# Kernel optimization log

Hardware: AMD Instinct MI355X
Metric: run time of the kernel (lower is better)

Reference implementation:

```python
import jax, jax.numpy as jnp
import numpy as np

B, S, E = 2, 2048, 1024
H = 16
HD = E // H  # 64


def setup_inputs() -> dict:
    key = jax.random.key(0)
    ks = jax.random.split(key, 9)
    sc = 1.0 / np.sqrt(E)
    return {
        "X": jax.random.normal(ks[0], (B, S, E), jnp.float32),
        "Wq": jax.random.normal(ks[1], (E, E), jnp.float32) * sc,
        "bq": jax.random.normal(ks[2], (E,), jnp.float32) * sc,
        "Wk": jax.random.normal(ks[3], (E, E), jnp.float32) * sc,
        "bk": jax.random.normal(ks[4], (E,), jnp.float32) * sc,
        "Wv": jax.random.normal(ks[5], (E, E), jnp.float32) * sc,
        "bv": jax.random.normal(ks[6], (E,), jnp.float32) * sc,
        "Wo": jax.random.normal(ks[7], (E, E), jnp.float32) * sc,
        "bo": jax.random.normal(ks[8], (E,), jnp.float32) * sc,
    }


def reference(X, Wq, bq, Wk, bk, Wv, bv, Wo, bo):
    b, s, e = X.shape
    # torch Linear: x @ W.T + b (weights stored (out, in))
    Q = X @ Wq.T + bq
    K = X @ Wk.T + bk
    V = X @ Wv.T + bv
    # (b, s, E) -> (b, H, s, HD)
    Q = Q.reshape(b, s, H, HD).transpose(0, 2, 1, 3)
    K = K.reshape(b, s, H, HD).transpose(0, 2, 1, 3)
    V = V.reshape(b, s, H, HD).transpose(0, 2, 1, 3)
    scores = jnp.einsum("bhqd,bhkd->bhqk", Q, K) / np.sqrt(HD).astype(np.float32)
    attn = jax.nn.softmax(scores, axis=-1)
    ctx = jnp.einsum("bhqk,bhkd->bhqd", attn, V)  # (b, H, s, HD)
    # Faithful to original: reshape (b,H,s,HD) -> (b,s,E) WITHOUT permuting heads back
    ctx = ctx.reshape(b, s, e)
    return ctx @ Wo.T + bo
```

## Files before the change

kernel.cpp:

```cpp
#include <hip/hip_runtime.h>


typedef __bf16 bf16x8 __attribute__((ext_vector_type(8)));
typedef __bf16 bf16x4 __attribute__((ext_vector_type(4)));
typedef float f32x4 __attribute__((ext_vector_type(4)));
typedef unsigned short ushort_t;

#define S_LEN 2048
#define E_DIM 1024
#define H_NUM 16
#define HD_DIM 64

__device__ __forceinline__ ushort_t f2bf(float f) {
  union { float f; unsigned u; } v; v.f = f;
  unsigned u = v.u;
  unsigned r = (u + 0x7FFFu + ((u >> 16) & 1u)) >> 16;
  return (ushort_t)r;
}

#define GLDS16(gp, lp)                                              \
  __builtin_amdgcn_global_load_lds(                                 \
      (const __attribute__((address_space(1))) unsigned int*)(gp),  \
      (__attribute__((address_space(3))) unsigned int*)(lp), 16, 0, 0)

__global__ __launch_bounds__(256) void cvt_all(
    const float* __restrict__ X, const float* __restrict__ Wq,
    const float* __restrict__ Wk, const float* __restrict__ Wv,
    const float* __restrict__ Wo, ushort_t* __restrict__ Xbf,
    ushort_t* __restrict__ Wqkv, ushort_t* __restrict__ Wob) {
  int i = blockIdx.x * 256 + threadIdx.x;
  const float* src;
  ushort_t* dst;
  int off;
  if (i < 1048576) {
    src = X; dst = Xbf; off = i;
  } else if (i < 1310720) {
    src = Wq; dst = Wqkv; off = i - 1048576;
  } else if (i < 1572864) {
    src = Wk; dst = Wqkv + (1 << 20); off = i - 1310720;
  } else if (i < 1835008) {
    src = Wv; dst = Wqkv + (2 << 20); off = i - 1572864;
  } else {
    src = Wo; dst = Wob; off = i - 1835008;
  }
  float4 v = ((const float4*)src)[off];
  ushort4 o;
  o.x = f2bf(v.x); o.y = f2bf(v.y); o.z = f2bf(v.z); o.w = f2bf(v.w);
  ((ushort4*)dst)[off] = o;
}

__global__ __launch_bounds__(256) void gemm_qkv(
    const ushort_t* __restrict__ Xbf, const ushort_t* __restrict__ Wqkv,
    const float* __restrict__ bq, const float* __restrict__ bk,
    const float* __restrict__ bv,
    ushort_t* __restrict__ Qb, ushort_t* __restrict__ Kb,
    ushort_t* __restrict__ Vt) {
  __shared__ ushort_t As[128 * 64];
  __shared__ ushort_t Bs[128 * 64];
  const int t = threadIdx.x;
  const int w = t >> 6, lane = t & 63, quad = lane >> 4, lr = lane & 15;
  const int m0 = blockIdx.y * 128, n0 = blockIdx.x * 128;
  const int wm = (w & 1) * 64, wn = (w >> 1) * 64;
  const int matid = n0 >> 10;
  const int nl0 = n0 & 1023;

  const int srow = t >> 3;
  const int gsrc = (t & 7) ^ (srow & 7);
  const ushort_t* Ag = Xbf + (size_t)(m0 + srow) * E_DIM + gsrc * 8;
  const ushort_t* Bg = Wqkv + (size_t)matid * E_DIM * E_DIM +
                       (size_t)(nl0 + srow) * E_DIM + gsrc * 8;

  f32x4 acc[4][4] = {};

  for (int kt = 0; kt < E_DIM / 64; ++kt) {
#pragma unroll
    for (int r = 0; r < 4; r++) {
      GLDS16(Ag + (size_t)r * 32 * E_DIM, As + r * 2048 + t * 8);
      GLDS16(Bg + (size_t)r * 32 * E_DIM, Bs + r * 2048 + t * 8);
    }
    Ag += 64; Bg += 64;
    __syncthreads();
#pragma unroll
    for (int kk = 0; kk < 2; kk++) {
      bf16x8 af[4], bfr[4];
      const int gs0 = (kk * 4 + quad) ^ (lr & 7);
#pragma unroll
      for (int i = 0; i < 4; i++) {
        af[i]  = *(const bf16x8*)(As + (wm + i * 16 + lr) * 64 + gs0 * 8);
        bfr[i] = *(const bf16x8*)(Bs + (wn + i * 16 + lr) * 64 + gs0 * 8);
      }
#pragma unroll
      for (int i = 0; i < 4; i++)
#pragma unroll
        for (int j = 0; j < 4; j++)
          acc[i][j] = __builtin_amdgcn_mfma_f32_16x16x32_bf16(
              af[i], bfr[j], acc[i][j], 0, 0, 0);
    }
    __syncthreads();
  }

  const float* bias_p = (matid == 0) ? bq : (matid == 1) ? bk : bv;
  if (matid < 2) {
    ushort_t* dst = (matid == 0) ? Qb : Kb;
    const float scl = (matid == 0) ? 0.125f : 1.0f;
#pragma unroll
    for (int j = 0; j < 4; j++) {
      int cl = (n0 + wn + j * 16 + lr) & 1023;
      int h = cl >> 6, d = cl & 63;
      float bias = bias_p[cl];
#pragma unroll
      for (int i = 0; i < 4; i++) {
#pragma unroll
        for (int r = 0; r < 4; r++) {
          int row = m0 + wm + i * 16 + quad * 4 + r;
          int bb = row >> 11, ss = row & 2047;
          size_t o = ((size_t)((bb * H_NUM + h) * S_LEN + ss)) * HD_DIM + d;
          dst[o] = f2bf((acc[i][j][r] + bias) * scl);
        }
      }
    }
  } else {
#pragma unroll
    for (int j = 0; j < 4; j++) {
      int cl = (n0 + wn + j * 16 + lr) & 1023;
      int h = cl >> 6, d = cl & 63;
      float bias = bias_p[cl];
#pragma unroll
      for (int i = 0; i < 4; i++) {
#pragma unroll
        for (int r = 0; r < 4; r++) {
          int row = m0 + wm + i * 16 + quad * 4 + r;
          int bb = row >> 11, ss = row & 2047;
          size_t o = ((size_t)((bb * H_NUM + h) * HD_DIM + d)) * S_LEN +
                     (ss & ~63) + ((ss & 15) * 4) + ((ss >> 4) & 3);
          Vt[o] = f2bf(acc[i][j][r] + bias);
        }
      }
    }
  }
}

__global__ __launch_bounds__(256) void attn(
    const ushort_t* __restrict__ Qb, const ushort_t* __restrict__ Kb,
    const ushort_t* __restrict__ Vt, ushort_t* __restrict__ Ctx) {
  __shared__ ushort_t Ks[64 * 64];
  __shared__ ushort_t Vs[64 * 64];
  __shared__ ushort_t Ps[64 * 72];
  const int t = threadIdx.x, w = t >> 6, lane = t & 63;
  const int quad = lane >> 4, lr = lane & 15;
  const int bh = blockIdx.y, q0 = blockIdx.x * 64;
  const ushort_t* Qg = Qb + ((size_t)bh * S_LEN + q0) * HD_DIM;
  const ushort_t* Kg = Kb + (size_t)bh * S_LEN * HD_DIM;
  const ushort_t* Vg = Vt + (size_t)bh * HD_DIM * S_LEN;

  const int srow = t >> 3;
  const int gsrc = (t & 7) ^ (srow & 7);

#pragma unroll
  for (int r = 0; r < 2; r++) {
    GLDS16(Qg + (size_t)(r * 32 + srow) * HD_DIM + gsrc * 8,
           Ps + r * 2048 + t * 8);
    GLDS16(Kg + (size_t)(r * 32 + srow) * HD_DIM + gsrc * 8,
           Ks + r * 2048 + t * 8);
    GLDS16(Vg + (size_t)(r * 32 + srow) * S_LEN + gsrc * 8,
           Vs + r * 2048 + t * 8);
  }
  __syncthreads();
  bf16x8 qf[2];
#pragma unroll
  for (int kc = 0; kc < 2; kc++) {
    int gs = (kc * 4 + quad) ^ (lr & 7);
    qf[kc] = *(const bf16x8*)(Ps + (w * 16 + lr) * 64 + gs * 8);
  }

  bf16x8 ones;
#pragma unroll
  for (int e = 0; e < 8; e++) ones[e] = (__bf16)1.0f;

  f32x4 cacc[4] = {};
  f32x4 lsum = {};

  for (int kt = 0; kt < S_LEN / 64; ++kt) {
    f32x4 sacc[4] = {};
#pragma unroll
    for (int nt = 0; nt < 4; nt++) {
#pragma unroll
      for (int kc = 0; kc < 2; kc++) {
        int gs = (kc * 4 + quad) ^ (lr & 7);
        bf16x8 kf = *(const bf16x8*)(Ks + (nt * 16 + lr) * 64 + gs * 8);
        sacc[nt] = __builtin_amdgcn_mfma_f32_16x16x32_bf16(
            qf[kc], kf, sacc[nt], 0, 0, 0);
      }
    }
    __syncthreads();

    {
      const int kn = (kt + 1) & (S_LEN / 64 - 1);
#pragma unroll
      for (int r = 0; r < 2; r++)
        GLDS16(Kg + (size_t)(kn * 64 + r * 32 + srow) * HD_DIM + gsrc * 8,
               Ks + r * 2048 + t * 8);
    }

#pragma unroll
    for (int i = 0; i < 4; i++) {
      float p0 = __expf(sacc[0][i]);
      float p1 = __expf(sacc[1][i]);
      float p2 = __expf(sacc[2][i]);
      float p3 = __expf(sacc[3][i]);
      bf16x4 pv;
      pv[0] = (__bf16)p0; pv[1] = (__bf16)p1;
      pv[2] = (__bf16)p2; pv[3] = (__bf16)p3;
      int row = w * 16 + quad * 4 + i;
      *(bf16x4*)(Ps + row * 72 + lr * 4) = pv;
    }

#pragma unroll
    for (int kc = 0; kc < 2; kc++) {
      bf16x8 pf =
          *(const bf16x8*)(Ps + (w * 16 + lr) * 72 + kc * 32 + quad * 8);
      lsum = __builtin_amdgcn_mfma_f32_16x16x32_bf16(pf, ones, lsum, 0, 0, 0);
#pragma unroll
      for (int dt = 0; dt < 4; dt++) {
        int gs = (kc * 4 + quad) ^ (lr & 7);
        bf16x8 vf = *(const bf16x8*)(Vs + (dt * 16 + lr) * 64 + gs * 8);
        cacc[dt] = __builtin_amdgcn_mfma_f32_16x16x32_bf16(
            pf, vf, cacc[dt], 0, 0, 0);
      }
    }
    __syncthreads();

    {
      const int kn = (kt + 1) & (S_LEN / 64 - 1);
#pragma unroll
      for (int r = 0; r < 2; r++)
        GLDS16(Vg + (size_t)(r * 32 + srow) * S_LEN + kn * 64 + gsrc * 8,
               Vs + r * 2048 + t * 8);
    }
  }

#pragma unroll
  for (int i = 0; i < 4; i++) {
    float inv = 1.0f / lsum[i];
    int srow2 = q0 + w * 16 + quad * 4 + i;
#pragma unroll
    for (int dt = 0; dt < 4; dt++)
      Ctx[((size_t)bh * S_LEN + srow2) * HD_DIM + dt * 16 + lr] =
          f2bf(cacc[dt][i] * inv);
  }
}

__global__ __launch_bounds__(256) void gemm_out(
    const ushort_t* __restrict__ Cb, const ushort_t* __restrict__ Wob,
    const float* __restrict__ bo, float* __restrict__ out) {
  __shared__ ushort_t As[64 * 64];
  __shared__ ushort_t Bs[64 * 64];
  const int t = threadIdx.x;
  const int w = t >> 6, lane = t & 63, quad = lane >> 4, lr = lane & 15;
  const int m0 = blockIdx.y * 64, n0 = blockIdx.x * 64;
  const int wm = (w & 1) * 32, wn = (w >> 1) * 32;

  const int srow = t >> 3;
  const int gsrc = (t & 7) ^ (srow & 7);
  const ushort_t* Ag = Cb + (size_t)(m0 + srow) * E_DIM + gsrc * 8;
  const ushort_t* Bg = Wob + (size_t)(n0 + srow) * E_DIM + gsrc * 8;

  f32x4 acc[2][2] = {};

  for (int kt = 0; kt < E_DIM / 64; ++kt) {
#pragma unroll
    for (int r = 0; r < 2; r++) {
      GLDS16(Ag + (size_t)r * 32 * E_DIM, As + r * 2048 + t * 8);
      GLDS16(Bg + (size_t)r * 32 * E_DIM, Bs + r * 2048 + t * 8);
    }
    Ag += 64; Bg += 64;
    __syncthreads();
#pragma unroll
    for (int kk = 0; kk < 2; kk++) {
      bf16x8 af[2], bfr[2];
      const int gs0 = (kk * 4 + quad) ^ (lr & 7);
#pragma unroll
      for (int i = 0; i < 2; i++) {
        af[i]  = *(const bf16x8*)(As + (wm + i * 16 + lr) * 64 + gs0 * 8);
        bfr[i] = *(const bf16x8*)(Bs + (wn + i * 16 + lr) * 64 + gs0 * 8);
      }
#pragma unroll
      for (int i = 0; i < 2; i++)
#pragma unroll
        for (int j = 0; j < 2; j++)
          acc[i][j] = __builtin_amdgcn_mfma_f32_16x16x32_bf16(
              af[i], bfr[j], acc[i][j], 0, 0, 0);
    }
    __syncthreads();
  }

#pragma unroll
  for (int j = 0; j < 2; j++) {
    int col = n0 + wn + j * 16 + lr;
    float bias = bo[col];
#pragma unroll
    for (int i = 0; i < 2; i++) {
#pragma unroll
      for (int r = 0; r < 4; r++) {
        int row = m0 + wm + i * 16 + quad * 4 + r;
        out[(size_t)row * E_DIM + col] = acc[i][j][r] + bias;
      }
    }
  }
}

extern "C" void kernel_launch(void* const* d_in, const int* in_sizes, int n_in,
                              void* d_out, int out_size, void* d_ws,
                              size_t ws_size, hipStream_t stream) {
  const float* X  = (const float*)d_in[0];
  const float* bq = (const float*)d_in[2];
  const float* bk = (const float*)d_in[4];
  const float* bv = (const float*)d_in[6];
  const float* Wo = (const float*)d_in[7];
  const float* bo = (const float*)d_in[8];
  float* out = (float*)d_out;

  char* ws = (char*)d_ws;
  ushort_t* Xbf  = (ushort_t*)(ws);
  ushort_t* Wqkv = (ushort_t*)(ws + ((size_t)8 << 20));
  ushort_t* Wob  = (ushort_t*)(ws + ((size_t)14 << 20));
  ushort_t* Qb   = (ushort_t*)(ws + ((size_t)16 << 20));
  ushort_t* Kb   = (ushort_t*)(ws + ((size_t)24 << 20));
  ushort_t* Vt   = (ushort_t*)(ws + ((size_t)32 << 20));
  ushort_t* Cb   = (ushort_t*)(ws + ((size_t)40 << 20));

  cvt_all<<<8192, 256, 0, stream>>>(X, (const float*)d_in[1],
                                    (const float*)d_in[3],
                                    (const float*)d_in[5], Wo, Xbf, Wqkv, Wob);

  gemm_qkv<<<dim3(24, 32), 256, 0, stream>>>(Xbf, Wqkv, bq, bk, bv, Qb, Kb, Vt);
  attn<<<dim3(32, 32), 256, 0, stream>>>(Qb, Kb, Vt, Cb);
  gemm_out<<<dim3(16, 64), 256, 0, stream>>>(Cb, Wob, bo, out);
}
```

Baseline: 196.2 us.

## Stage QKV epilogue through LDS, enlarge attention and out-proj tiles, use exp2

The QKV GEMM epilogue now writes results into shared memory with swizzling, then emits 16-byte coalesced global stores for Q/K and transposed V instead of scalar 2-byte scatters. Q/K use swapped MFMA operands to fit this layout. The attention kernel processes 128 query rows per block, so each K/V tile is reused across two row tiles. It also folds log2(e) into the Q scale so it can use a native exp2. The output GEMM tile grows to 128x64. These changes cut store traffic and K/V reloads but raise register and LDS pressure and halve the number of blocks in the attention and out-proj grids.

```diff
diff --git a/kernel.cpp b/kernel.cpp
--- a/kernel.cpp
+++ b/kernel.cpp
@@ -10,6 +10,12 @@
 #define E_DIM 1024
 #define H_NUM 16
 #define HD_DIM 64
+
+#if __has_builtin(__builtin_amdgcn_exp2f)
+#define EXP2(x) __builtin_amdgcn_exp2f(x)
+#else
+#define EXP2(x) __exp2f(x)
+#endif
 
 __device__ __forceinline__ ushort_t f2bf(float f) {
   union { float f; unsigned u; } v; v.f = f;
@@ -55,8 +61,9 @@
     const float* __restrict__ bv,
     ushort_t* __restrict__ Qb, ushort_t* __restrict__ Kb,
     ushort_t* __restrict__ Vt) {
-  __shared__ ushort_t As[128 * 64];
-  __shared__ ushort_t Bs[128 * 64];
+  __shared__ ushort_t smem[16384];
+  ushort_t* As = smem;
+  ushort_t* Bs = smem + 8192;
   const int t = threadIdx.x;
   const int w = t >> 6, lane = t & 63, quad = lane >> 4, lr = lane & 15;
   const int m0 = blockIdx.y * 128, n0 = blockIdx.x * 128;
@@ -89,53 +96,90 @@
         af[i]  = *(const bf16x8*)(As + (wm + i * 16 + lr) * 64 + gs0 * 8);
         bfr[i] = *(const bf16x8*)(Bs + (wn + i * 16 + lr) * 64 + gs0 * 8);
       }
-#pragma unroll
-      for (int i = 0; i < 4; i++)
-#pragma unroll
-        for (int j = 0; j < 4; j++)
-          acc[i][j] = __builtin_amdgcn_mfma_f32_16x16x32_bf16(
-              af[i], bfr[j], acc[i][j], 0, 0, 0);
+      if (matid < 2) {
+#pragma unroll
+        for (int i = 0; i < 4; i++)
+#pragma unroll
+          for (int j = 0; j < 4; j++)
+            acc[i][j] = __builtin_amdgcn_mfma_f32_16x16x32_bf16(
+                bfr[j], af[i], acc[i][j], 0, 0, 0);
+      } else {
+#pragma unroll
+        for (int i = 0; i < 4; i++)
+#pragma unroll
+          for (int j = 0; j < 4; j++)
+            acc[i][j] = __builtin_amdgcn_mfma_f32_16x16x32_bf16(
+                af[i], bfr[j], acc[i][j], 0, 0, 0);
+      }
     }
     __syncthreads();
   }
 
   const float* bias_p = (matid == 0) ? bq : (matid == 1) ? bk : bv;
+  ushort_t* Ls = smem;
   if (matid < 2) {
     ushort_t* dst = (matid == 0) ? Qb : Kb;
-    const float scl = (matid == 0) ? 0.125f : 1.0f;
+    const float scl = (matid == 0) ? 0.18033688f : 1.0f;
 #pragma unroll
     for (int j = 0; j < 4; j++) {
-      int cl = (n0 + wn + j * 16 + lr) & 1023;
-      int h = cl >> 6, d = cl & 63;
-      float bias = bias_p[cl];
+      const int nb = wn + j * 16 + quad * 4;
+      float b0 = bias_p[nl0 + nb], b1 = bias_p[nl0 + nb + 1];
+      float b2 = bias_p[nl0 + nb + 2], b3 = bias_p[nl0 + nb + 3];
 #pragma unroll
       for (int i = 0; i < 4; i++) {
-#pragma unroll
-        for (int r = 0; r < 4; r++) {
-          int row = m0 + wm + i * 16 + quad * 4 + r;
-          int bb = row >> 11, ss = row & 2047;
-          size_t o = ((size_t)((bb * H_NUM + h) * S_LEN + ss)) * HD_DIM + d;
-          dst[o] = f2bf((acc[i][j][r] + bias) * scl);
-        }
-      }
+        const int m = wm + i * 16 + lr;
+        bf16x4 pv;
+        pv[0] = (__bf16)((acc[i][j][0] + b0) * scl);
+        pv[1] = (__bf16)((acc[i][j][1] + b1) * scl);
+        pv[2] = (__bf16)((acc[i][j][2] + b2) * scl);
+        pv[3] = (__bf16)((acc[i][j][3] + b3) * scl);
+        *(bf16x4*)(Ls + m * 128 + (((nb >> 3) ^ (m & 7)) * 8) + (nb & 7)) = pv;
+      }
+    }
+    __syncthreads();
+#pragma unroll
+    for (int it = 0; it < 8; it++) {
+      const int task = t + 256 * it;
+      const int m = task >> 4, g = task & 15;
+      uint4 val = *(const uint4*)(Ls + m * 128 + ((g ^ (m & 7)) * 8));
+      const int s = m0 + m, bb = s >> 11, ss = s & 2047;
+      const int cl = nl0 + g * 8, h = cl >> 6, dd = cl & 63;
+      *(uint4*)(dst + ((size_t)((bb * H_NUM + h) * S_LEN + ss)) * HD_DIM + dd) =
+          val;
     }
   } else {
 #pragma unroll
     for (int j = 0; j < 4; j++) {
-      int cl = (n0 + wn + j * 16 + lr) & 1023;
-      int h = cl >> 6, d = cl & 63;
-      float bias = bias_p[cl];
+      const int n = wn + j * 16 + lr;
+      const float bias = bias_p[nl0 + n];
 #pragma unroll
       for (int i = 0; i < 4; i++) {
-#pragma unroll
-        for (int r = 0; r < 4; r++) {
-          int row = m0 + wm + i * 16 + quad * 4 + r;
-          int bb = row >> 11, ss = row & 2047;
-          size_t o = ((size_t)((bb * H_NUM + h) * HD_DIM + d)) * S_LEN +
-                     (ss & ~63) + ((ss & 15) * 4) + ((ss >> 4) & 3);
-          Vt[o] = f2bf(acc[i][j][r] + bias);
-        }
-      }
+        const int mb = wm + i * 16 + quad * 4;
+        bf16x4 pv;
+        pv[0] = (__bf16)(acc[i][j][0] + bias);
+        pv[1] = (__bf16)(acc[i][j][1] + bias);
+        pv[2] = (__bf16)(acc[i][j][2] + bias);
+        pv[3] = (__bf16)(acc[i][j][3] + bias);
+        *(bf16x4*)(Ls + n * 128 + (((mb >> 3) ^ (n & 7)) * 8) + (mb & 7)) = pv;
+      }
+    }
+    __syncthreads();
+    const int n = t & 127, grp = t >> 7;
+    ushort_t v[64];
+#pragma unroll
+    for (int c = 0; c < 8; c++)
+      *(uint4*)(v + c * 8) =
+          *(const uint4*)(Ls + n * 128 + (((grp * 8 + c) ^ (n & 7)) * 8));
+    const int cl = nl0 + n, h = cl >> 6, dd = cl & 63;
+    const int sgb = m0 + grp * 64, bb = sgb >> 11, ssb = sgb & 2047;
+    ushort_t* dstp =
+        Vt + ((size_t)((bb * H_NUM + h) * HD_DIM + dd)) * S_LEN + ssb;
+#pragma unroll
+    for (int q = 0; q < 8; q++) {
+      ushort_t o8[8];
+#pragma unroll
+      for (int u = 0; u < 8; u++) o8[u] = v[16 * (u & 3) + 2 * q + (u >> 2)];
+      *(uint4*)(dstp + q * 8) = *(const uint4*)o8;
     }
   }
 }
@@ -145,10 +189,10 @@
     const ushort_t* __restrict__ Vt, ushort_t* __restrict__ Ctx) {
   __shared__ ushort_t Ks[64 * 64];
   __shared__ ushort_t Vs[64 * 64];
-  __shared__ ushort_t Ps[64 * 72];
+  __shared__ ushort_t Ps[128 * 72];
   const int t = threadIdx.x, w = t >> 6, lane = t & 63;
   const int quad = lane >> 4, lr = lane & 15;
-  const int bh = blockIdx.y, q0 = blockIdx.x * 64;
+  const int bh = blockIdx.y, q0 = blockIdx.x * 128;
   const ushort_t* Qg = Qb + ((size_t)bh * S_LEN + q0) * HD_DIM;
   const ushort_t* Kg = Kb + (size_t)bh * S_LEN * HD_DIM;
   const ushort_t* Vg = Vt + (size_t)bh * HD_DIM * S_LEN;
@@ -157,135 +201,151 @@
   const int gsrc = (t & 7) ^ (srow & 7);
 
 #pragma unroll
-  for (int r = 0; r < 2; r++) {
+  for (int r = 0; r < 4; r++)
     GLDS16(Qg + (size_t)(r * 32 + srow) * HD_DIM + gsrc * 8,
            Ps + r * 2048 + t * 8);
+#pragma unroll
+  for (int r = 0; r < 2; r++) {
     GLDS16(Kg + (size_t)(r * 32 + srow) * HD_DIM + gsrc * 8,
            Ks + r * 2048 + t * 8);
     GLDS16(Vg + (size_t)(r * 32 + srow) * S_LEN + gsrc * 8,
            Vs + r * 2048 + t * 8);
   }
   __syncthreads();
-  bf16x8 qf[2];
-#pragma unroll
-  for (int kc = 0; kc < 2; kc++) {
-    int gs = (kc * 4 + quad) ^ (lr & 7);
-    qf[kc] = *(const bf16x8*)(Ps + (w * 16 + lr) * 64 + gs * 8);
-  }
+  bf16x8 qf[2][2];
+#pragma unroll
+  for (int mt = 0; mt < 2; mt++)
+#pragma unroll
+    for (int kc = 0; kc < 2; kc++) {
+      int gs = (kc * 4 + quad) ^ (lr & 7);
+      qf[mt][kc] =
+          *(const bf16x8*)(Ps + (w * 32 + mt * 16 + lr) * 64 + gs * 8);
+    }
 
   bf16x8 ones;
 #pragma unroll
   for (int e = 0; e < 8; e++) ones[e] = (__bf16)1.0f;
 
-  f32x4 cacc[4] = {};
-  f32x4 lsum = {};
+  f32x4 cacc[2][4] = {};
+  f32x4 lsum[2] = {};
 
   for (int kt = 0; kt < S_LEN / 64; ++kt) {
-    f32x4 sacc[4] = {};
+    f32x4 sacc[2][4] = {};
 #pragma unroll
     for (int nt = 0; nt < 4; nt++) {
 #pragma unroll
       for (int kc = 0; kc < 2; kc++) {
         int gs = (kc * 4 + quad) ^ (lr & 7);
         bf16x8 kf = *(const bf16x8*)(Ks + (nt * 16 + lr) * 64 + gs * 8);
-        sacc[nt] = __builtin_amdgcn_mfma_f32_16x16x32_bf16(
-            qf[kc], kf, sacc[nt], 0, 0, 0);
-      }
-    }
-    __syncthreads();
-
-    {
-      const int kn = (kt + 1) & (S_LEN / 64 - 1);
-#pragma unroll
-      for (int r = 0; r < 2; r++)
-        GLDS16(Kg + (size_t)(kn * 64 + r * 32 + srow) * HD_DIM + gsrc * 8,
-               Ks + r * 2048 + t * 8);
-    }
-
+        sacc[0][nt] = __builtin_amdgcn_mfma_f32_16x16x32_bf16(
+            qf[0][kc], kf, sacc[0][nt], 0, 0, 0);
+        sacc[1][nt] = __builtin_amdgcn_mfma_f32_16x16x32_bf16(
+            qf[1][kc], kf, sacc[1][nt], 0, 0, 0);
+      }
+    }
+    __syncthreads();
+
+    const int kn = (kt + 1) & (S_LEN / 64 - 1);
+#pragma unroll
+    for (int r = 0; r < 2; r++)
+      GLDS16(Kg + (size_t)(kn * 64 + r * 32 + srow) * HD_DIM + gsrc * 8,
+             Ks + r * 2048 + t * 8);
+
+#pragma unroll
+    for (int mt = 0; mt < 2; mt++) {
+#pragma unroll
+      for (int i = 0; i < 4; i++) {
+        float p0 = EXP2(sacc[mt][0][i]);
+        float p1 = EXP2(sacc[mt][1][i]);
+        float p2 = EXP2(sacc[mt][2][i]);
+        float p3 = EXP2(sacc[mt][3][i]);
+        bf16x4 pv;
+        pv[0] = (__bf16)p0; pv[1] = (__bf16)p1;
+        pv[2] = (__bf16)p2; pv[3] = (__bf16)p3;
+        int row = w * 32 + mt * 16 + quad * 4 + i;
+        *(bf16x4*)(Ps + row * 72 + lr * 4) = pv;
+      }
+    }
+
+#pragma unroll
+    for (int kc = 0; kc < 2; kc++) {
+      int gs = (kc * 4 + quad) ^ (lr & 7);
+      bf16x8 vf[4];
+#pragma unroll
+      for (int dt = 0; dt < 4; dt++)
+        vf[dt] = *(const bf16x8*)(Vs + (dt * 16 + lr) * 64 + gs * 8);
+#pragma unroll
+      for (int mt = 0; mt < 2; mt++) {
+        bf16x8 pf = *(const bf16x8*)(Ps + (w * 32 + mt * 16 + lr) * 72 +
+                                     kc * 32 + quad * 8);
+        lsum[mt] =
+            __builtin_amdgcn_mfma_f32_16x16x32_bf16(pf, ones, lsum[mt], 0, 0, 0);
+#pragma unroll
+        for (int dt = 0; dt < 4; dt++)
+          cacc[mt][dt] = __builtin_amdgcn_mfma_f32_16x16x32_bf16(
+              pf, vf[dt], cacc[mt][dt], 0, 0, 0);
+      }
+    }
+    __syncthreads();
+
+#pragma unroll
+    for (int r = 0; r < 2; r++)
+      GLDS16(Vg + (size_t)(r * 32 + srow) * S_LEN + kn * 64 + gsrc * 8,
+             Vs + r * 2048 + t * 8);
+  }
+
+#pragma unroll
+  for (int mt = 0; mt < 2; mt++) {
 #pragma unroll
     for (int i = 0; i < 4; i++) {
-      float p0 = __expf(sacc[0][i]);
-      float p1 = __expf(sacc[1][i]);
-      float p2 = __expf(sacc[2][i]);
-      float p3 = __expf(sacc[3][i]);
-      bf16x4 pv;
-      pv[0] = (__bf16)p0; pv[1] = (__bf16)p1;
-      pv[2] = (__bf16)p2; pv[3] = (__bf16)p3;
-      int row = w * 16 + quad * 4 + i;
-      *(bf16x4*)(Ps + row * 72 + lr * 4) = pv;
-    }
-
-#pragma unroll
-    for (int kc = 0; kc < 2; kc++) {
-      bf16x8 pf =
-          *(const bf16x8*)(Ps + (w * 16 + lr) * 72 + kc * 32 + quad * 8);
-      lsum = __builtin_amdgcn_mfma_f32_16x16x32_bf16(pf, ones, lsum, 0, 0, 0);
-#pragma unroll
-      for (int dt = 0; dt < 4; dt++) {
-        int gs = (kc * 4 + quad) ^ (lr & 7);
-        bf16x8 vf = *(const bf16x8*)(Vs + (dt * 16 + lr) * 64 + gs * 8);
-        cacc[dt] = __builtin_amdgcn_mfma_f32_16x16x32_bf16(
-            pf, vf, cacc[dt], 0, 0, 0);
-      }
-    }
-    __syncthreads();
-
-    {
-      const int kn = (kt + 1) & (S_LEN / 64 - 1);
-#pragma unroll
-      for (int r = 0; r < 2; r++)
-        GLDS16(Vg + (size_t)(r * 32 + srow) * S_LEN + kn * 64 + gsrc * 8,
-               Vs + r * 2048 + t * 8);
-    }
-  }
-
-#pragma unroll
-  for (int i = 0; i < 4; i++) {
-    float inv = 1.0f / lsum[i];
-    int srow2 = q0 + w * 16 + quad * 4 + i;
-#pragma unroll
-    for (int dt = 0; dt < 4; dt++)
-      Ctx[((size_t)bh * S_LEN + srow2) * HD_DIM + dt * 16 + lr] =
-          f2bf(cacc[dt][i] * inv);
+      float inv = 1.0f / lsum[mt][i];
+      int srow2 = q0 + w * 32 + mt * 16 + quad * 4 + i;
+#pragma unroll
+      for (int dt = 0; dt < 4; dt++)
+        Ctx[((size_t)bh * S_LEN + srow2) * HD_DIM + dt * 16 + lr] =
+            f2bf(cacc[mt][dt][i] * inv);
+    }
   }
 }
 
 __global__ __launch_bounds__(256) void gemm_out(
     const ushort_t* __restrict__ Cb, const ushort_t* __restrict__ Wob,
     const float* __restrict__ bo, float* __restrict__ out) {
-  __shared__ ushort_t As[64 * 64];
+  __shared__ ushort_t As[128 * 64];
   __shared__ ushort_t Bs[64 * 64];
   const int t = threadIdx.x;
   const int w = t >> 6, lane = t & 63, quad = lane >> 4, lr = lane & 15;
-  const int m0 = blockIdx.y * 64, n0 = blockIdx.x * 64;
-  const int wm = (w & 1) * 32, wn = (w >> 1) * 32;
+  const int m0 = blockIdx.y * 128, n0 = blockIdx.x * 64;
+  const int wm = (w & 1) * 64, wn = (w >> 1) * 32;
 
   const int srow = t >> 3;
   const int gsrc = (t & 7) ^ (srow & 7);
   const ushort_t* Ag = Cb + (size_t)(m0 + srow) * E_DIM + gsrc * 8;
   const ushort_t* Bg = Wob + (size_t)(n0 + srow) * E_DIM + gsrc * 8;
 
-  f32x4 acc[2][2] = {};
+  f32x4 acc[4][2] = {};
 
   for (int kt = 0; kt < E_DIM / 64; ++kt) {
 #pragma unroll
-    for (int r = 0; r < 2; r++) {
+    for (int r = 0; r < 4; r++)
       GLDS16(Ag + (size_t)r * 32 * E_DIM, As + r * 2048 + t * 8);
+#pragma unroll
+    for (int r = 0; r < 2; r++)
       GLDS16(Bg + (size_t)r * 32 * E_DIM, Bs + r * 2048 + t * 8);
-    }
     Ag += 64; Bg += 64;
     __syncthreads();
 #pragma unroll
     for (int kk = 0; kk < 2; kk++) {
-      bf16x8 af[2], bfr[2];
+      bf16x8 af[4], bfr[2];
       const int gs0 = (kk * 4 + quad) ^ (lr & 7);
 #pragma unroll
-      for (int i = 0; i < 2; i++) {
-        af[i]  = *(const bf16x8*)(As + (wm + i * 16 + lr) * 64 + gs0 * 8);
-        bfr[i] = *(const bf16x8*)(Bs + (wn + i * 16 + lr) * 64 + gs0 * 8);
-      }
-#pragma unroll
-      for (int i = 0; i < 2; i++)
+      for (int i = 0; i < 4; i++)
+        af[i] = *(const bf16x8*)(As + (wm + i * 16 + lr) * 64 + gs0 * 8);
+#pragma unroll
+      for (int j = 0; j < 2; j++)
+        bfr[j] = *(const bf16x8*)(Bs + (wn + j * 16 + lr) * 64 + gs0 * 8);
+#pragma unroll
+      for (int i = 0; i < 4; i++)
 #pragma unroll
         for (int j = 0; j < 2; j++)
           acc[i][j] = __builtin_amdgcn_mfma_f32_16x16x32_bf16(
@@ -299,7 +359,7 @@
     int col = n0 + wn + j * 16 + lr;
     float bias = bo[col];
 #pragma unroll
-    for (int i = 0; i < 2; i++) {
+    for (int i = 0; i < 4; i++) {
 #pragma unroll
       for (int r = 0; r < 4; r++) {
         int row = m0 + wm + i * 16 + quad * 4 + r;
@@ -334,6 +394,6 @@
                                     (const float*)d_in[5], Wo, Xbf, Wqkv, Wob);
 
   gemm_qkv<<<dim3(24, 32), 256, 0, stream>>>(Xbf, Wqkv, bq, bk, bv, Qb, Kb, Vt);
-  attn<<<dim3(32, 32), 256, 0, stream>>>(Qb, Kb, Vt, Cb);
-  gemm_out<<<dim3(16, 64), 256, 0, stream>>>(Cb, Wob, bo, out);
-}
+  attn<<<dim3(16, 32), 256, 0, stream>>>(Qb, Kb, Vt, Cb);
+  gemm_out<<<dim3(16, 32), 256, 0, stream>>>(Cb, Wob, bo, out);
+}
```

After: 195.4 us. About the same (-0.4%).
